# Kernel optimization log

Measured on AMD Instinct MI355X. Metric: run time of the kernel, lower is better.

Reference implementation:

```python
import jax, jax.numpy as jnp
import numpy as np

B, S, D, H = 2, 4096, 512, 8
HD = D // H
SCALE = float(np.sqrt(HD))


def setup_inputs() -> dict:
    key = jax.random.key(0)
    ks = jax.random.split(key, 11)
    std = 1.0 / np.sqrt(D)
    inp = {
        "query": jax.random.normal(ks[0], (B, S, D), jnp.float32),
        "key": jax.random.normal(ks[1], (B, S, D), jnp.float32),
        "value": jax.random.normal(ks[2], (B, S, D), jnp.float32),
        "Wq": jax.random.normal(ks[3], (D, D), jnp.float32) * std,
        "bq": jnp.zeros((D,), jnp.float32),
        "Wk": jax.random.normal(ks[4], (D, D), jnp.float32) * std,
        "bk": jnp.zeros((D,), jnp.float32),
        "Wv": jax.random.normal(ks[5], (D, D), jnp.float32) * std,
        "bv": jnp.zeros((D,), jnp.float32),
        "Wo": jax.random.normal(ks[6], (D, D), jnp.float32) * std,
        "bo": jnp.zeros((D,), jnp.float32),
    }
    return inp


def reference(query, key, value, Wq, bq, Wk, bk, Wv, bv, Wo, bo):
    # Linear projections, split into heads: [B, H, S, HD]
    def proj(x, W, b):
        y = jnp.einsum('bsd,df->bsf', x, W) + b
        return y.reshape(B, -1, H, HD).transpose(0, 2, 1, 3)

    Q = proj(query, Wq, bq)
    K = proj(key, Wk, bk)
    V = proj(value, Wv, bv)

    # Full [B, H, S, S] score matrix (faithful to the naive original)
    scores = jnp.einsum('bhqd,bhkd->bhqk', Q, K) / SCALE
    attn = jax.nn.softmax(scores, axis=-1)  # dropout = identity in eval
    attended = jnp.einsum('bhqk,bhkd->bhqd', attn, V)
    attended = attended.transpose(0, 2, 1, 3).reshape(B, -1, D)
    return jnp.einsum('bsd,df->bsf', attended, Wo) + bo
```

## Files before the change

### kernel.cpp

```cpp
#include <hip/hip_runtime.h>

typedef short short8 __attribute__((ext_vector_type(8)));
typedef short short4v __attribute__((ext_vector_type(4)));
typedef float f32x4 __attribute__((ext_vector_type(4)));
typedef float f32x16 __attribute__((ext_vector_type(16)));
typedef unsigned uint2v __attribute__((ext_vector_type(2)));

typedef __attribute__((address_space(1))) void gvoid;
typedef __attribute__((address_space(3))) void lvoid;

#define DEV static __device__ __forceinline__

constexpr int Dm = 512;
constexpr int Sm = 4096;
constexpr int Hh = 8;

#define QSCALE 0.18033688011112042f

DEV short f2bf(float f) {
  union { float f; unsigned u; } v; v.f = f;
  unsigned r = v.u + 0x7FFFu + ((v.u >> 16) & 1u);
  return (short)(r >> 16);
}

DEV float exp2_fast(float x) {
#if __has_builtin(__builtin_amdgcn_exp2f)
  return __builtin_amdgcn_exp2f(x);
#else
  return exp2f(x);
#endif
}

DEV float max3f(float a, float b, float c) { return fmaxf(fmaxf(a, b), c); }

DEV unsigned cvt_pk_bf16(float lo, float hi) {
  unsigned r;
  asm("v_cvt_pk_bf16_f32 %0, %1, %2" : "=v"(r) : "v"(lo), "v"(hi));
  return r;
}

DEV uint2v pl32swap(unsigned a, unsigned b) {
  return __builtin_amdgcn_permlane32_swap(a, b, false, false);
}
DEV float swap_max(float x) { return fmaxf(x, __shfl_xor(x, 32, 64)); }
DEV float swap_add(float x) { return x + __shfl_xor(x, 32, 64); }

DEV void async16(const void* g, void* l) {
  __builtin_amdgcn_global_load_lds((gvoid*)g, (lvoid*)l, 16, 0, 0);
}

__global__ __launch_bounds__(256) void cast_qkv(
    const float* __restrict__ q, const float* __restrict__ k,
    const float* __restrict__ v, short* __restrict__ xq,
    short* __restrict__ xk, short* __restrict__ xv) {
  int t = blockIdx.y;
  const float* src = (t == 0) ? q : (t == 1) ? k : v;
  short* dst = (t == 0) ? xq : (t == 1) ? xk : xv;
  long i = (long)(blockIdx.x * 256 + threadIdx.x) * 4;
  float4 f = *(const float4*)(src + i);
  short4v o;
  o[0] = f2bf(f.x); o[1] = f2bf(f.y); o[2] = f2bf(f.z); o[3] = f2bf(f.w);
  *(short4v*)(dst + i) = o;
}

__global__ __launch_bounds__(256) void wtrans(
    const float* __restrict__ wq, const float* __restrict__ wk,
    const float* __restrict__ wv, const float* __restrict__ wo,
    short* __restrict__ wt) {
  __shared__ short T[64 * 72];
  const int tid = threadIdx.x;
  const int n0 = blockIdx.x * 64, k0 = blockIdx.y * 64, w = blockIdx.z;
  const float* W = (w == 0) ? wq : (w == 1) ? wk : (w == 2) ? wv : wo;
  for (int t = 0; t < 4; ++t) {
    int flat = t * 256 + tid;
    int r = flat >> 4, c4 = flat & 15;
    float4 f = *(const float4*)(W + (k0 + r) * 512 + n0 + c4 * 4);
    T[(c4 * 4 + 0) * 72 + r] = f2bf(f.x);
    T[(c4 * 4 + 1) * 72 + r] = f2bf(f.y);
    T[(c4 * 4 + 2) * 72 + r] = f2bf(f.z);
    T[(c4 * 4 + 3) * 72 + r] = f2bf(f.w);
  }
  __syncthreads();
  for (int t = 0; t < 2; ++t) {
    int flat = t * 256 + tid;
    int r = flat >> 3, c = flat & 7;
    short8 v = *(const short8*)(T + r * 72 + c * 8);
    *(short8*)(wt + ((long)w << 18) + (n0 + r) * 512 + k0 + c * 8) = v;
  }
}

__global__ __launch_bounds__(256) void vtrans(
    const short* __restrict__ V, short* __restrict__ VT) {
  __shared__ short T[64 * 72];
  const int tid = threadIdx.x;
  const int s0 = blockIdx.x * 64, d0 = blockIdx.y * 64, b = blockIdx.z;
  for (int t = 0; t < 2; ++t) {
    int flat = t * 256 + tid;
    int sl = flat >> 3, c = flat & 7;
    short8 v = *(const short8*)(V + ((long)b * Sm + s0 + sl) * Dm + d0 + c * 8);
    for (int j = 0; j < 8; ++j) T[(c * 8 + j) * 72 + sl] = v[j];
  }
  __syncthreads();
  for (int t = 0; t < 2; ++t) {
    int flat = t * 256 + tid;
    int dl = flat >> 3, c = flat & 7;
    short8 v = *(const short8*)(T + dl * 72 + c * 8);
    *(short8*)(VT + ((long)b * Dm + d0 + dl) * Sm + s0 + c * 8) = v;
  }
}

template <bool OUT_BF16>
DEV void gemm_body(const short* __restrict__ A, const short* __restrict__ Bt,
                   const float* __restrict__ bias, float scale,
                   void* __restrict__ Yv, short* As, short* Bs) {
  constexpr int K = 512, N = 512, BK = 64;
  const int tid = threadIdx.x, lane = tid & 63, w = tid >> 6;
  const int lm = lane & 15, lg = lane >> 4;
  const int wr = w >> 1, wc = w & 1;
  const long bm = (long)blockIdx.y * 128;
  const long bn = (long)blockIdx.x * 128;
  f32x4 zero = {0.f, 0.f, 0.f, 0.f};
  f32x4 acc[4][4];
  for (int m = 0; m < 4; ++m)
    for (int n = 0; n < 4; ++n) acc[m][n] = zero;
  for (int k0 = 0; k0 < K; k0 += BK) {
    __syncthreads();
    for (int t = 0; t < 4; ++t) {
      int flat = t * 256 + tid;
      int row = flat >> 3, c = flat & 7;
      async16(A + (bm + row) * K + k0 + ((c ^ (row & 7)) * 8), As + flat * 8);
    }
    for (int t = 0; t < 4; ++t) {
      int flat = t * 256 + tid;
      int row = flat >> 3, c = flat & 7;
      async16(Bt + (bn + row) * K + k0 + ((c ^ (row & 7)) * 8), Bs + flat * 8);
    }
    __syncthreads();
    for (int kk = 0; kk < 2; ++kk) {
      short8 a[4], b[4];
      for (int m = 0; m < 4; ++m)
        a[m] = *(const short8*)(As + (wr * 64 + m * 16 + lm) * BK +
                                ((kk * 4 + lg) ^ (lm & 7)) * 8);
      for (int n = 0; n < 4; ++n)
        b[n] = *(const short8*)(Bs + (wc * 64 + n * 16 + lm) * BK +
                                ((kk * 4 + lg) ^ (lm & 7)) * 8);
      for (int m = 0; m < 4; ++m)
        for (int n = 0; n < 4; ++n)
          acc[m][n] = __builtin_amdgcn_mfma_f32_16x16x32_bf16(a[m], b[n], acc[m][n], 0, 0, 0);
    }
  }
  for (int m = 0; m < 4; ++m)
    for (int n = 0; n < 4; ++n) {
      long row0 = bm + wr * 64 + m * 16 + lg * 4;
      int col = (int)bn + wc * 64 + n * 16 + lm;
      float bb = bias[col];
      for (int j = 0; j < 4; ++j) {
        float val = (acc[m][n][j] + bb) * scale;
        if (OUT_BF16)
          ((short*)Yv)[(row0 + j) * N + col] = f2bf(val);
        else
          ((float*)Yv)[(row0 + j) * N + col] = val;
      }
    }
}

__global__ __launch_bounds__(256) void gemm_proj(
    const short* __restrict__ Xq, const short* __restrict__ Xk,
    const short* __restrict__ Xv, const short* __restrict__ Wt,
    const float* __restrict__ bq, const float* __restrict__ bk,
    const float* __restrict__ bv, short* __restrict__ Qb,
    short* __restrict__ Kb, short* __restrict__ Vb) {
  __shared__ short As[128 * 64];
  __shared__ short Bs[128 * 64];
  int z = blockIdx.z;
  const short* A = (z == 0) ? Xq : (z == 1) ? Xk : Xv;
  const short* Bt = Wt + (long)z * 512 * 512;
  const float* bias = (z == 0) ? bq : (z == 1) ? bk : bv;
  short* Y = (z == 0) ? Qb : (z == 1) ? Kb : Vb;
  float scale = (z == 0) ? QSCALE : 1.f;
  gemm_body<true>(A, Bt, bias, scale, Y, As, Bs);
}

__global__ __launch_bounds__(256) void gemm_out(
    const short* __restrict__ A, const short* __restrict__ Bt,
    const float* __restrict__ bias, float* __restrict__ Y) {
  __shared__ short As[128 * 64];
  __shared__ short Bs[128 * 64];
  gemm_body<false>(A, Bt, bias, 1.f, Y, As, Bs);
}

__global__ __launch_bounds__(256) void attn(
    const short* __restrict__ Qb, const short* __restrict__ Kb,
    const short* __restrict__ VTb, float* __restrict__ Op0,
    float* __restrict__ Op1, float2* __restrict__ Ml) {
  __shared__ short Ks[2][64 * 64];
  __shared__ short Vt[2][64 * 64];
  const int tid = threadIdx.x, lane = tid & 63, w = tid >> 6;
  const int q32 = lane & 31, l5 = lane >> 5;
  const int bh = blockIdx.y, b = bh >> 3, h = bh & 7;
  const int z = blockIdx.z;
  const int kvbase = z * (Sm / 2);
  const long baseQ = (long)b * Sm * Dm + h * 64;
  const long baseVT = ((long)b * Dm + h * 64) * Sm;
  const int q0w = blockIdx.x * 128 + w * 32;

  short8 qf[4];
#pragma unroll
  for (int ks = 0; ks < 4; ++ks)
    qf[ks] = *(const short8*)(Qb + baseQ + (long)(q0w + q32) * Dm + ks * 16 + l5 * 8);

  f32x16 o0, o1;
#pragma unroll
  for (int r = 0; r < 16; ++r) { o0[r] = 0.f; o1[r] = 0.f; }
  float mrun = -1e30f, lrun = 0.f;

  const int r0 = tid >> 3, c0 = tid & 7;
  const int r1 = 32 + (tid >> 3);
  const short* gk0 = Kb + baseQ + (long)(kvbase + r0) * Dm + (c0 ^ (r0 & 7)) * 8;
  const short* gk1 = Kb + baseQ + (long)(kvbase + r1) * Dm + (c0 ^ (r1 & 7)) * 8;
  const short* gv0 = VTb + baseVT + (long)r0 * Sm + kvbase + (c0 ^ (r0 & 7)) * 8;
  const short* gv1 = VTb + baseVT + (long)r1 * Sm + kvbase + (c0 ^ (r1 & 7)) * 8;
  const int l0 = tid * 8, l1 = (256 + tid) * 8;

  async16(gk0, &Ks[0][l0]); async16(gk1, &Ks[0][l1]);
  async16(gv0, &Vt[0][l0]); async16(gv1, &Vt[0][l1]);
  gk0 += 64 * Dm; gk1 += 64 * Dm; gv0 += 64; gv1 += 64;
  __syncthreads();

  const int cxor = q32 & 7;

  constexpr int NTILES = Sm / 2 / 64;
  for (int it = 0; it < NTILES; ++it) {
    const int cur = it & 1;
    if (it + 1 < NTILES) {
      async16(gk0, &Ks[cur ^ 1][l0]); async16(gk1, &Ks[cur ^ 1][l1]);
      async16(gv0, &Vt[cur ^ 1][l0]); async16(gv1, &Vt[cur ^ 1][l1]);
      gk0 += 64 * Dm; gk1 += 64 * Dm; gv0 += 64; gv1 += 64;
    }

    f32x16 sc0, sc1;
#pragma unroll
    for (int r = 0; r < 16; ++r) { sc0[r] = 0.f; sc1[r] = 0.f; }
    __builtin_amdgcn_s_setprio(1);
#pragma unroll
    for (int ks = 0; ks < 4; ++ks) {
      int cx = (2 * ks + l5) ^ cxor;
      short8 kf0 = *(const short8*)(&Ks[cur][q32 * 64 + cx * 8]);
      short8 kf1 = *(const short8*)(&Ks[cur][(32 + q32) * 64 + cx * 8]);
      sc0 = __builtin_amdgcn_mfma_f32_32x32x16_bf16(kf0, qf[ks], sc0, 0, 0, 0);
      sc1 = __builtin_amdgcn_mfma_f32_32x32x16_bf16(kf1, qf[ks], sc1, 0, 0, 0);
    }
    __builtin_amdgcn_s_setprio(0);

    float t1 = max3f(sc0[0], sc0[1], sc0[2]);
    float t2 = max3f(sc0[3], sc0[4], sc0[5]);
    float t3 = max3f(sc0[6], sc0[7], sc0[8]);
    float t4 = max3f(sc0[9], sc0[10], sc0[11]);
    float t5 = max3f(sc0[12], sc0[13], sc0[14]);
    float ma = max3f(max3f(t1, t2, t3), max3f(t4, t5, sc0[15]), sc1[0]);
    t1 = max3f(sc1[1], sc1[2], sc1[3]);
    t2 = max3f(sc1[4], sc1[5], sc1[6]);
    t3 = max3f(sc1[7], sc1[8], sc1[9]);
    t4 = max3f(sc1[10], sc1[11], sc1[12]);
    t5 = max3f(sc1[13], sc1[14], sc1[15]);
    float tmax = fmaxf(ma, max3f(max3f(t1, t2, t3), t4, t5));
    tmax = swap_max(tmax);

    float mi = fmaxf(mrun, tmax);
    float cc = exp2_fast(mrun - mi);
    mrun = mi;
    lrun *= cc;
#pragma unroll
    for (int r = 0; r < 16; ++r) {
      float ccr = __shfl(cc, ((r & 3) + 8 * (r >> 2)) + 4 * l5, 32);
      o0[r] *= ccr;
      o1[r] *= ccr;
    }

    float la = 0.f, lb = 0.f;
#pragma unroll
    for (int r = 0; r < 16; ++r) {
      sc0[r] = exp2_fast(sc0[r] - mrun); la += sc0[r];
      sc1[r] = exp2_fast(sc1[r] - mrun); lb += sc1[r];
    }
    lrun += la + lb;

    __builtin_amdgcn_s_setprio(1);
#pragma unroll
    for (int kc = 0; kc < 4; ++kc) {
      const f32x16& sch = (kc < 2) ? sc0 : sc1;
      const int bb = 8 * (kc & 1);
      unsigned A = cvt_pk_bf16(sch[bb + 0], sch[bb + 1]);
      unsigned B = cvt_pk_bf16(sch[bb + 2], sch[bb + 3]);
      unsigned C = cvt_pk_bf16(sch[bb + 4], sch[bb + 5]);
      unsigned D = cvt_pk_bf16(sch[bb + 6], sch[bb + 7]);
      uint2v rac = pl32swap(A, C);
      uint2v rbd = pl32swap(B, D);
      union { unsigned u[4]; short8 s; } pu;
      pu.u[0] = rac[0]; pu.u[1] = rbd[0]; pu.u[2] = rac[1]; pu.u[3] = rbd[1];
      int cx = (2 * kc + l5) ^ cxor;
      short8 vf0 = *(const short8*)(&Vt[cur][q32 * 64 + cx * 8]);
      short8 vf1 = *(const short8*)(&Vt[cur][(32 + q32) * 64 + cx * 8]);
      o0 = __builtin_amdgcn_mfma_f32_32x32x16_bf16(pu.s, vf0, o0, 0, 0, 0);
      o1 = __builtin_amdgcn_mfma_f32_32x32x16_bf16(pu.s, vf1, o1, 0, 0, 0);
    }
    __builtin_amdgcn_s_setprio(0);
    __syncthreads();
  }

  lrun = swap_add(lrun);

  float* Op = (z == 0) ? Op0 : Op1;
#pragma unroll
  for (int r = 0; r < 16; ++r) {
    int q = (r & 3) + 8 * (r >> 2) + 4 * l5;
    long rowoff = baseQ + (long)(q0w + q) * Dm;
    Op[rowoff + q32] = o0[r];
    Op[rowoff + 32 + q32] = o1[r];
  }
  if (l5 == 0) {
    float2 ml; ml.x = mrun; ml.y = lrun;
    Ml[(long)(z * 16 + bh) * Sm + q0w + q32] = ml;
  }
}

__global__ __launch_bounds__(256) void merge2(
    const float* __restrict__ Op0, const float* __restrict__ Op1,
    const float2* __restrict__ Ml, short* __restrict__ Ob) {
  long idx = (long)blockIdx.x * 256 + threadIdx.x;
  long row = idx >> 6;
  int c8 = (int)(idx & 63);
  int col = c8 * 8;
  int h = col >> 6;
  int b = (int)(row >> 12);
  int s = (int)(row & 4095);
  int bh = b * 8 + h;
  float2 ml0 = Ml[(long)(0 * 16 + bh) * Sm + s];
  float2 ml1 = Ml[(long)(1 * 16 + bh) * Sm + s];
  float M = fmaxf(ml0.x, ml1.x);
  float w0 = exp2_fast(ml0.x - M), w1 = exp2_fast(ml1.x - M);
  float dn = 1.0f / (ml0.y * w0 + ml1.y * w1);
  w0 *= dn; w1 *= dn;
  long off = row * 512 + col;
  float4 a0 = *(const float4*)(Op0 + off);
  float4 a1 = *(const float4*)(Op0 + off + 4);
  float4 b0 = *(const float4*)(Op1 + off);
  float4 b1 = *(const float4*)(Op1 + off + 4);
  short8 o;
  o[0] = f2bf(a0.x * w0 + b0.x * w1);
  o[1] = f2bf(a0.y * w0 + b0.y * w1);
  o[2] = f2bf(a0.z * w0 + b0.z * w1);
  o[3] = f2bf(a0.w * w0 + b0.w * w1);
  o[4] = f2bf(a1.x * w0 + b1.x * w1);
  o[5] = f2bf(a1.y * w0 + b1.y * w1);
  o[6] = f2bf(a1.z * w0 + b1.z * w1);
  o[7] = f2bf(a1.w * w0 + b1.w * w1);
  *(short8*)(Ob + off) = o;
}

extern "C" void kernel_launch(void* const* d_in, const int* in_sizes, int n_in,
                              void* d_out, int out_size, void* d_ws, size_t ws_size,
                              hipStream_t stream) {
  const float* query = (const float*)d_in[0];
  const float* key_  = (const float*)d_in[1];
  const float* value = (const float*)d_in[2];
  const float* Wq = (const float*)d_in[3]; const float* bq = (const float*)d_in[4];
  const float* Wk = (const float*)d_in[5]; const float* bk = (const float*)d_in[6];
  const float* Wv = (const float*)d_in[7]; const float* bv = (const float*)d_in[8];
  const float* Wo = (const float*)d_in[9]; const float* bo = (const float*)d_in[10];

  const long NT = (long)2 * Sm * Dm;
  short* Xq = (short*)d_ws;
  short* Xk = Xq + NT;
  short* Xv = Xk + NT;
  short* Wt = Xv + NT;
  short* Qb = Wt + 4 * 512 * 512;
  short* Kb = Qb + NT;
  short* Vb = Kb + NT;
  short* VT = Xv;
  float* Op0 = (float*)d_ws;
  float* Op1 = (float*)(Vb + NT);
  float2* Ml = (float2*)(Op1 + NT);
  short* Ob = Vb;

  cast_qkv<<<dim3(4096, 3), 256, 0, stream>>>(query, key_, value, Xq, Xk, Xv);
  wtrans<<<dim3(8, 8, 4), 256, 0, stream>>>(Wq, Wk, Wv, Wo, Wt);

  gemm_proj<<<dim3(4, 64, 3), 256, 0, stream>>>(Xq, Xk, Xv, Wt, bq, bk, bv,
                                                Qb, Kb, Vb);

  vtrans<<<dim3(Sm / 64, Dm / 64, 2), 256, 0, stream>>>(Vb, VT);

  attn<<<dim3(Sm / 128, 2 * Hh, 2), 256, 0, stream>>>(Qb, Kb, VT, Op0, Op1, Ml);

  merge2<<<dim3((2 * Sm * 512 / 8) / 256), 256, 0, stream>>>(Op0, Op1, Ml, Ob);

  gemm_out<<<dim3(4, 64), 256, 0, stream>>>(Ob, Wt + 3L * 512 * 512, bo,
                                            (float*)d_out);
}
```

Baseline: 192.2 us.

## Split KV across four blocks when workspace allows, add lazy softmax rescale

The attention kernel becomes templated on the number of KV splits and uses four splits when the workspace is large enough, giving 512 blocks instead of 256 for better occupancy across the CUs. The merge kernel is generalized to combine N partial outputs. Separately, the online-softmax rescale of the accumulators is skipped unless some row's max grows by more than 8 (log2 units), which removes shuffles and multiplies on most tiles. The cost is more fp32 partial-output traffic for the extra splits, and the lazy rescale lets exponentials grow up to 2^8 before correction.

```diff
diff --git a/kernel.cpp b/kernel.cpp
--- a/kernel.cpp
+++ b/kernel.cpp
@@ -14,6 +14,7 @@
 constexpr int Dm = 512;
 constexpr int Sm = 4096;
 constexpr int Hh = 8;
+constexpr long NTe = (long)2 * Sm * Dm;
 
 #define QSCALE 0.18033688011112042f
 
@@ -189,17 +190,19 @@
   gemm_body<false>(A, Bt, bias, 1.f, Y, As, Bs);
 }
 
+template <int NSPLIT>
 __global__ __launch_bounds__(256) void attn(
     const short* __restrict__ Qb, const short* __restrict__ Kb,
     const short* __restrict__ VTb, float* __restrict__ Op0,
-    float* __restrict__ Op1, float2* __restrict__ Ml) {
+    float* __restrict__ OpRest, float2* __restrict__ Ml) {
   __shared__ short Ks[2][64 * 64];
   __shared__ short Vt[2][64 * 64];
   const int tid = threadIdx.x, lane = tid & 63, w = tid >> 6;
   const int q32 = lane & 31, l5 = lane >> 5;
   const int bh = blockIdx.y, b = bh >> 3, h = bh & 7;
   const int z = blockIdx.z;
-  const int kvbase = z * (Sm / 2);
+  constexpr int KVLEN = Sm / NSPLIT;
+  const int kvbase = z * KVLEN;
   const long baseQ = (long)b * Sm * Dm + h * 64;
   const long baseVT = ((long)b * Dm + h * 64) * Sm;
   const int q0w = blockIdx.x * 128 + w * 32;
@@ -229,7 +232,7 @@
 
   const int cxor = q32 & 7;
 
-  constexpr int NTILES = Sm / 2 / 64;
+  constexpr int NTILES = KVLEN / 64;
   for (int it = 0; it < NTILES; ++it) {
     const int cur = it & 1;
     if (it + 1 < NTILES) {
@@ -266,15 +269,17 @@
     float tmax = fmaxf(ma, max3f(max3f(t1, t2, t3), t4, t5));
     tmax = swap_max(tmax);
 
-    float mi = fmaxf(mrun, tmax);
-    float cc = exp2_fast(mrun - mi);
-    mrun = mi;
-    lrun *= cc;
-#pragma unroll
-    for (int r = 0; r < 16; ++r) {
-      float ccr = __shfl(cc, ((r & 3) + 8 * (r >> 2)) + 4 * l5, 32);
-      o0[r] *= ccr;
-      o1[r] *= ccr;
+    if (__any(tmax > mrun + 8.f)) {
+      float mi = fmaxf(mrun, tmax);
+      float cc = exp2_fast(mrun - mi);
+      mrun = mi;
+      lrun *= cc;
+#pragma unroll
+      for (int r = 0; r < 16; ++r) {
+        float ccr = __shfl(cc, ((r & 3) + 8 * (r >> 2)) + 4 * l5, 32);
+        o0[r] *= ccr;
+        o1[r] *= ccr;
+      }
     }
 
     float la = 0.f, lb = 0.f;
@@ -310,7 +315,7 @@
 
   lrun = swap_add(lrun);
 
-  float* Op = (z == 0) ? Op0 : Op1;
+  float* Op = (z == 0) ? Op0 : OpRest + (long)(z - 1) * NTe;
 #pragma unroll
   for (int r = 0; r < 16; ++r) {
     int q = (r & 3) + 8 * (r >> 2) + 4 * l5;
@@ -324,8 +329,9 @@
   }
 }
 
-__global__ __launch_bounds__(256) void merge2(
-    const float* __restrict__ Op0, const float* __restrict__ Op1,
+template <int NSPLIT>
+__global__ __launch_bounds__(256) void mergeN(
+    const float* __restrict__ Op0, const float* __restrict__ OpRest,
     const float2* __restrict__ Ml, short* __restrict__ Ob) {
   long idx = (long)blockIdx.x * 256 + threadIdx.x;
   long row = idx >> 6;
@@ -335,26 +341,37 @@
   int b = (int)(row >> 12);
   int s = (int)(row & 4095);
   int bh = b * 8 + h;
-  float2 ml0 = Ml[(long)(0 * 16 + bh) * Sm + s];
-  float2 ml1 = Ml[(long)(1 * 16 + bh) * Sm + s];
-  float M = fmaxf(ml0.x, ml1.x);
-  float w0 = exp2_fast(ml0.x - M), w1 = exp2_fast(ml1.x - M);
-  float dn = 1.0f / (ml0.y * w0 + ml1.y * w1);
-  w0 *= dn; w1 *= dn;
+  float2 ml[NSPLIT];
+  float M = -3e38f;
+#pragma unroll
+  for (int z = 0; z < NSPLIT; ++z) {
+    ml[z] = Ml[(long)(z * 16 + bh) * Sm + s];
+    M = fmaxf(M, ml[z].x);
+  }
+  float wz[NSPLIT], den = 0.f;
+#pragma unroll
+  for (int z = 0; z < NSPLIT; ++z) {
+    wz[z] = exp2_fast(ml[z].x - M);
+    den += ml[z].y * wz[z];
+  }
+  float inv = 1.0f / den;
   long off = row * 512 + col;
-  float4 a0 = *(const float4*)(Op0 + off);
-  float4 a1 = *(const float4*)(Op0 + off + 4);
-  float4 b0 = *(const float4*)(Op1 + off);
-  float4 b1 = *(const float4*)(Op1 + off + 4);
+  float acc[8];
+#pragma unroll
+  for (int i = 0; i < 8; ++i) acc[i] = 0.f;
+#pragma unroll
+  for (int z = 0; z < NSPLIT; ++z) {
+    const float* Op = (z == 0) ? Op0 : OpRest + (long)(z - 1) * NTe;
+    float4 a0 = *(const float4*)(Op + off);
+    float4 a1 = *(const float4*)(Op + off + 4);
+    acc[0] += a0.x * wz[z]; acc[1] += a0.y * wz[z];
+    acc[2] += a0.z * wz[z]; acc[3] += a0.w * wz[z];
+    acc[4] += a1.x * wz[z]; acc[5] += a1.y * wz[z];
+    acc[6] += a1.z * wz[z]; acc[7] += a1.w * wz[z];
+  }
   short8 o;
-  o[0] = f2bf(a0.x * w0 + b0.x * w1);
-  o[1] = f2bf(a0.y * w0 + b0.y * w1);
-  o[2] = f2bf(a0.z * w0 + b0.z * w1);
-  o[3] = f2bf(a0.w * w0 + b0.w * w1);
-  o[4] = f2bf(a1.x * w0 + b1.x * w1);
-  o[5] = f2bf(a1.y * w0 + b1.y * w1);
-  o[6] = f2bf(a1.z * w0 + b1.z * w1);
-  o[7] = f2bf(a1.w * w0 + b1.w * w1);
+#pragma unroll
+  for (int i = 0; i < 8; ++i) o[i] = f2bf(acc[i] * inv);
   *(short8*)(Ob + off) = o;
 }
 
@@ -369,19 +386,22 @@
   const float* Wv = (const float*)d_in[7]; const float* bv = (const float*)d_in[8];
   const float* Wo = (const float*)d_in[9]; const float* bo = (const float*)d_in[10];
 
-  const long NT = (long)2 * Sm * Dm;
   short* Xq = (short*)d_ws;
-  short* Xk = Xq + NT;
-  short* Xv = Xk + NT;
-  short* Wt = Xv + NT;
+  short* Xk = Xq + NTe;
+  short* Xv = Xk + NTe;
+  short* Wt = Xv + NTe;
   short* Qb = Wt + 4 * 512 * 512;
-  short* Kb = Qb + NT;
-  short* Vb = Kb + NT;
+  short* Kb = Qb + NTe;
+  short* Vb = Kb + NTe;
   short* VT = Xv;
   float* Op0 = (float*)d_ws;
-  float* Op1 = (float*)(Vb + NT);
-  float2* Ml = (float2*)(Op1 + NT);
+  float* OpRest = (float*)(Vb + NTe);
   short* Ob = Vb;
+
+  const size_t base_bytes = (size_t)(6 * NTe + 4 * 512 * 512) * 2;
+  const size_t need4 = base_bytes + 3 * (size_t)NTe * 4 + (size_t)4 * 16 * Sm * 8;
+  const int nsplit = (ws_size >= need4) ? 4 : 2;
+  float2* Ml = (float2*)(OpRest + (size_t)(nsplit - 1) * NTe);
 
   cast_qkv<<<dim3(4096, 3), 256, 0, stream>>>(query, key_, value, Xq, Xk, Xv);
   wtrans<<<dim3(8, 8, 4), 256, 0, stream>>>(Wq, Wk, Wv, Wo, Wt);
@@ -391,9 +411,17 @@
 
   vtrans<<<dim3(Sm / 64, Dm / 64, 2), 256, 0, stream>>>(Vb, VT);
 
-  attn<<<dim3(Sm / 128, 2 * Hh, 2), 256, 0, stream>>>(Qb, Kb, VT, Op0, Op1, Ml);
-
-  merge2<<<dim3((2 * Sm * 512 / 8) / 256), 256, 0, stream>>>(Op0, Op1, Ml, Ob);
+  if (nsplit == 4) {
+    attn<4><<<dim3(Sm / 128, 2 * Hh, 4), 256, 0, stream>>>(Qb, Kb, VT, Op0,
+                                                           OpRest, Ml);
+    mergeN<4><<<dim3((2 * Sm * 512 / 8) / 256), 256, 0, stream>>>(Op0, OpRest,
+                                                                  Ml, Ob);
+  } else {
+    attn<2><<<dim3(Sm / 128, 2 * Hh, 2), 256, 0, stream>>>(Qb, Kb, VT, Op0,
+                                                           OpRest, Ml);
+    mergeN<2><<<dim3((2 * Sm * 512 / 8) / 256), 256, 0, stream>>>(Op0, OpRest,
+                                                                  Ml, Ob);
+  }
 
   gemm_out<<<dim3(4, 64), 256, 0, stream>>>(Ob, Wt + 3L * 512 * 512, bo,
                                             (float*)d_out);
```

Measured after the change: 184.9 us. -3.8%, faster.
